# Kernel tuning notes

Measured on AMD Instinct MI355X. Metric: run time of the kernel, lower is better.

Reference implementation:

```python
import jax, jax.numpy as jnp
import numpy as np

N, E, CIN, H, B, NCOV, NCLASS, T = 50000, 800000, 64, 64, 256, 8, 2, 3


def setup_inputs() -> dict:
    key = jax.random.key(0)
    ks = jax.random.split(key, 24)
    s = 1.0 / np.sqrt(H)
    nrm = lambda k, shp, sc: (jax.random.normal(k, shp, jnp.float32) * sc)
    p = {}
    p["x"] = nrm(ks[0], (N, 3 * CIN), 1.0)
    p["edge_index"] = jax.random.randint(ks[1], (2, E), 0, N)
    p["cov"] = nrm(ks[2], (B, NCOV), 1.0)
    p["batch"] = jnp.sort(jax.random.randint(ks[3], (N,), 0, B))
    p["h0"] = nrm(ks[4], (B, H), 1.0)
    p["c0"] = nrm(ks[5], (B, H), 1.0)
    # GCNEncoder params (shared across the 3 channel slices, as in the torch code)
    p["lin_W"] = nrm(ks[6], (CIN, H), s)
    p["lin_b"] = jnp.zeros((H,), jnp.float32)
    p["conv1_W"] = nrm(ks[7], (H, H), s)
    p["conv1_b"] = jnp.zeros((H,), jnp.float32)
    p["conv2_W"] = nrm(ks[8], (H, H), s)
    p["conv2_b"] = jnp.zeros((H,), jnp.float32)
    # LSTM (1 layer), torch gate order i,f,g,o
    p["Wih"] = nrm(ks[9], (4 * H, H), s)
    p["Whh"] = nrm(ks[10], (4 * H, H), s)
    p["bih"] = jnp.zeros((4 * H,), jnp.float32)
    p["bhh"] = jnp.zeros((4 * H,), jnp.float32)
    p["w0_W"] = nrm(ks[11], (H, H), s)
    p["w0_b"] = jnp.zeros((H,), jnp.float32)
    p["attn_W"] = nrm(ks[12], (1, H), s)
    p["attn_b"] = jnp.zeros((1,), jnp.float32)
    p["l1_W"] = nrm(ks[13], (8, H), s)
    p["l1_b"] = jnp.zeros((8,), jnp.float32)
    p["l2_W"] = nrm(ks[14], (NCLASS, 8 + NCOV), 1.0 / np.sqrt(8 + NCOV))
    p["l2_b"] = jnp.zeros((NCLASS,), jnp.float32)
    return p


def _gcn_conv(x, src, dst, dinv, W, b):
    xw = x @ W
    norm = dinv[src] * dinv[dst]                      # [E]
    agg = jax.ops.segment_sum(norm[:, None] * xw[src], dst, num_segments=N)
    agg = agg + (2.0 * dinv * dinv)[:, None] * xw     # self-loop (weight 2)
    return agg + b


def _encoder(x, src, dst, dinv, lin_W, lin_b, c1W, c1b, c2W, c2b):
    out = x @ lin_W + lin_b                           # dropout = identity (eval)
    out1 = jax.nn.relu(_gcn_conv(out, src, dst, dinv, c1W, c1b)) + out
    out2 = _gcn_conv(out1, src, dst, dinv, c2W, c2b) + out1
    return out2


def reference(x, edge_index, cov, batch, h0, c0, lin_W, lin_b, conv1_W, conv1_b,
              conv2_W, conv2_b, Wih, Whh, bih, bhh, w0_W, w0_b, attn_W, attn_b,
              l1_W, l1_b, l2_W, l2_b):
    src, dst = edge_index[0], edge_index[1]
    deg = jax.ops.segment_sum(jnp.ones((E,), jnp.float32), dst, num_segments=N) + 2.0
    dinv = jax.lax.rsqrt(deg)
    enc = lambda xi: _encoder(xi, src, dst, dinv, lin_W, lin_b,
                              conv1_W, conv1_b, conv2_W, conv2_b)
    o1 = enc(x[:, :CIN]); o2 = enc(x[:, CIN:2 * CIN]); o3 = enc(x[:, 2 * CIN:])
    # global_mean_pool per branch
    cnt = jnp.maximum(jax.ops.segment_sum(jnp.ones((N,), jnp.float32), batch,
                                          num_segments=B), 1.0)[:, None]
    pool = lambda o: jax.ops.segment_sum(o, batch, num_segments=B) / cnt
    seq = jnp.stack([pool(o1), pool(o2), pool(o3)], axis=1)  # [B, 3, H]

    # 1-layer LSTM over T=3 (torch gate order i,f,g,o)
    def step(carry, x_t):
        h, c = carry
        g = x_t @ Wih.T + bih + h @ Whh.T + bhh
        i, f, gg, o = jnp.split(g, 4, axis=-1)
        c = jax.nn.sigmoid(f) * c + jax.nn.sigmoid(i) * jnp.tanh(gg)
        h = jax.nn.sigmoid(o) * jnp.tanh(c)
        return (h, c), h

    (_, _), hs = jax.lax.scan(step, (h0, c0), jnp.swapaxes(seq, 0, 1))
    rnn_out = jnp.swapaxes(hs, 0, 1)                         # [B, T, H]
    r = jnp.tanh(rnn_out @ w0_W.T + w0_b)
    attn = jax.nn.softmax((r @ attn_W.T + attn_b)[..., 0], axis=1)  # [B, T]
    pooled = jnp.einsum('bth,bt->bh', r, attn)
    out = jax.nn.relu(pooled @ l1_W.T + l1_b)
    out = jnp.concatenate([out, cov], axis=1)
    out = out @ l2_W.T + l2_b
    return attn, out
```

## Files before the change

### kernel.cpp

```cpp
#include <hip/hip_runtime.h>
#include <math.h>


#define TT 3
#define CHUNK 2048
#define BCAP 16384

typedef __attribute__((ext_vector_type(2))) float floatx2;

__device__ __forceinline__ float sigmoidf_(float x) { return 1.f / (1.f + expf(-x)); }

__global__ void brow_sorted(const int* __restrict__ batch, int* __restrict__ brow,
                            int N, int B) {
    int n = blockIdx.x * 256 + threadIdx.x;
    if (n >= N) return;
    int b = batch[n];
    if (n == 0) {
        for (int q = 0; q <= b; ++q) brow[q] = 0;
    } else {
        int pb = batch[n - 1];
        for (int q = pb + 1; q <= b; ++q) brow[q] = n;
    }
    if (n == N - 1) {
        for (int q = b + 1; q <= B; ++q) brow[q] = N;
    }
}

__global__ void stage_direct(const int* __restrict__ src, const int* __restrict__ dst,
                             int* __restrict__ bcnt, unsigned* __restrict__ stg, int E) {
    __shared__ int hcnt[256], hbase[256], hcur[256];
    hcnt[threadIdx.x] = 0;
    __syncthreads();
    int base = blockIdx.x * CHUNK;
    for (int i = threadIdx.x; i < CHUNK; i += 256) {
        int e = base + i;
        if (e < E) atomicAdd(&hcnt[dst[e] >> 8], 1);
    }
    __syncthreads();
    int c = hcnt[threadIdx.x];
    if (c) hbase[threadIdx.x] = atomicAdd(&bcnt[threadIdx.x], c);
    hcur[threadIdx.x] = 0;
    __syncthreads();
    for (int i = threadIdx.x; i < CHUNK; i += 256) {
        int e = base + i;
        if (e < E) {
            int d = dst[e];
            int b = d >> 8;
            int r = atomicAdd(&hcur[b], 1);
            stg[(long)b * BCAP + hbase[b] + r] =
                (unsigned)src[e] | ((unsigned)(d & 255) << 24);
        }
    }
}

__global__ void scan_buckets(const int* __restrict__ bcnt, int* __restrict__ boff,
                             int nb, int E) {
    __shared__ int s[256];
    int v = (threadIdx.x < nb) ? bcnt[threadIdx.x] : 0;
    s[threadIdx.x] = v;
    __syncthreads();
    for (int off = 1; off < 256; off <<= 1) {
        int t = (threadIdx.x >= off) ? s[threadIdx.x - off] : 0;
        __syncthreads();
        s[threadIdx.x] += t;
        __syncthreads();
    }
    if (threadIdx.x < nb) boff[threadIdx.x] = s[threadIdx.x] - v;
    if (threadIdx.x == 0) boff[nb] = E;
}

__global__ void bucket_build(const unsigned* __restrict__ stg, const int* __restrict__ bcnt,
                             const int* __restrict__ boff, int* __restrict__ rowptr,
                             float* __restrict__ dinv, int* __restrict__ csrc,
                             int N, int E) {
    const int b = blockIdx.x;
    const int n0 = b << 8;
    __shared__ int cnt[256];
    __shared__ int pfx[256];
    cnt[threadIdx.x] = 0;
    __syncthreads();
    const long s = (long)b * BCAP;
    const long e = s + bcnt[b];
    for (long p = s + threadIdx.x; p < e; p += 256)
        atomicAdd(&cnt[stg[p] >> 24], 1);
    __syncthreads();
    int v = cnt[threadIdx.x];
    pfx[threadIdx.x] = v;
    __syncthreads();
    for (int off = 1; off < 256; off <<= 1) {
        int t = (threadIdx.x >= off) ? pfx[threadIdx.x - off] : 0;
        __syncthreads();
        pfx[threadIdx.x] += t;
        __syncthreads();
    }
    int rowbase = boff[b] + pfx[threadIdx.x] - v;
    int n = n0 + threadIdx.x;
    if (n < N) {
        rowptr[n] = rowbase;
        dinv[n] = rsqrtf((float)v + 2.0f);
    }
    if (b == 0 && threadIdx.x == 0) rowptr[N] = E;
    cnt[threadIdx.x] = rowbase;
    __syncthreads();
    for (long p = s + threadIdx.x; p < e; p += 256) {
        unsigned u = stg[p];
        int dl = u >> 24;
        int r = atomicAdd(&cnt[dl], 1);
        csrc[r] = (int)(u & 0xFFFFFFu);
    }
}

__global__ __launch_bounds__(256) void gemm64_f32(
    const float* __restrict__ A, int lda, long aStride,
    const float* __restrict__ W, const float* __restrict__ bias,
    float* __restrict__ C, long cStride, int nrows) {
    __shared__ float AT[64][68];
    __shared__ float Ws[64][68];
    const int t = threadIdx.x;
    const float* Ab = A + (long)blockIdx.y * aStride;
    const int r0 = blockIdx.x * 64;

    #pragma unroll
    for (int i = 0; i < 4; ++i) {
        int idx = t + i * 256;
        int k = idx >> 4, c4 = idx & 15;
        *(float4*)&Ws[k][c4 * 4] = *(const float4*)(W + k * 64 + c4 * 4);
    }
    #pragma unroll
    for (int i = 0; i < 4; ++i) {
        int idx = t + i * 256;
        int row = idx >> 4, c4 = idx & 15;
        int gr = r0 + row;
        float4 a = make_float4(0.f, 0.f, 0.f, 0.f);
        if (gr < nrows) a = *(const float4*)(Ab + (long)gr * lda + c4 * 4);
        AT[c4 * 4 + 0][row] = a.x;
        AT[c4 * 4 + 1][row] = a.y;
        AT[c4 * 4 + 2][row] = a.z;
        AT[c4 * 4 + 3][row] = a.w;
    }
    __syncthreads();

    const int rowg = t >> 4, colg = t & 15;
    float acc[4][4] = {};
    #pragma unroll 8
    for (int k = 0; k < 64; ++k) {
        float4 av = *(const float4*)&AT[k][rowg * 4];
        float4 wv = *(const float4*)&Ws[k][colg * 4];
        #pragma unroll
        for (int i = 0; i < 4; ++i) {
            acc[i][0] = fmaf(((const float*)&av)[i], wv.x, acc[i][0]);
            acc[i][1] = fmaf(((const float*)&av)[i], wv.y, acc[i][1]);
            acc[i][2] = fmaf(((const float*)&av)[i], wv.z, acc[i][2]);
            acc[i][3] = fmaf(((const float*)&av)[i], wv.w, acc[i][3]);
        }
    }
    float b0 = bias[colg * 4 + 0], b1 = bias[colg * 4 + 1];
    float b2 = bias[colg * 4 + 2], b3 = bias[colg * 4 + 3];
    float* Cb = C + (long)blockIdx.y * cStride;
    #pragma unroll
    for (int i = 0; i < 4; ++i) {
        int gr = r0 + rowg * 4 + i;
        if (gr < nrows)
            *(float4*)(Cb + (long)gr * 64 + colg * 4) =
                make_float4(acc[i][0] + b0, acc[i][1] + b1, acc[i][2] + b2, acc[i][3] + b3);
    }
}

__global__ __launch_bounds__(256) void gemm64_t8(
    const float* __restrict__ A, long aStride, const float* __restrict__ W,
    unsigned* __restrict__ T8, const float* __restrict__ dinvp, int nrows) {
    __shared__ float AT[64][68];
    __shared__ float Ws[64][68];
    const int t = threadIdx.x;
    const float* Ab = A + (long)blockIdx.y * aStride;
    const int r0 = blockIdx.x * 64;

    #pragma unroll
    for (int i = 0; i < 4; ++i) {
        int idx = t + i * 256;
        int k = idx >> 4, c4 = idx & 15;
        *(float4*)&Ws[k][c4 * 4] = *(const float4*)(W + k * 64 + c4 * 4);
    }
    #pragma unroll
    for (int i = 0; i < 4; ++i) {
        int idx = t + i * 256;
        int row = idx >> 4, c4 = idx & 15;
        int gr = r0 + row;
        float4 a = make_float4(0.f, 0.f, 0.f, 0.f);
        if (gr < nrows) a = *(const float4*)(Ab + (long)gr * 64 + c4 * 4);
        AT[c4 * 4 + 0][row] = a.x;
        AT[c4 * 4 + 1][row] = a.y;
        AT[c4 * 4 + 2][row] = a.z;
        AT[c4 * 4 + 3][row] = a.w;
    }
    __syncthreads();

    const int rowg = t >> 4, colg = t & 15;
    float acc[4][4] = {};
    #pragma unroll 8
    for (int k = 0; k < 64; ++k) {
        float4 av = *(const float4*)&AT[k][rowg * 4];
        float4 wv = *(const float4*)&Ws[k][colg * 4];
        #pragma unroll
        for (int i = 0; i < 4; ++i) {
            acc[i][0] = fmaf(((const float*)&av)[i], wv.x, acc[i][0]);
            acc[i][1] = fmaf(((const float*)&av)[i], wv.y, acc[i][1]);
            acc[i][2] = fmaf(((const float*)&av)[i], wv.z, acc[i][2]);
            acc[i][3] = fmaf(((const float*)&av)[i], wv.w, acc[i][3]);
        }
    }
    #pragma unroll
    for (int i = 0; i < 4; ++i) {
        int gr = r0 + rowg * 4 + i;
        if (gr >= nrows) continue;
        float sc = dinvp[gr];
        int r = 0;
        r = __builtin_amdgcn_cvt_pk_fp8_f32(acc[i][0] * sc, acc[i][1] * sc, r, false);
        r = __builtin_amdgcn_cvt_pk_fp8_f32(acc[i][2] * sc, acc[i][3] * sc, r, true);
        T8[(long)gr * 48 + blockIdx.y * 16 + colg] = (unsigned)r;
    }
}

#define EDGE3(uu)                                                        \
    {                                                                    \
        floatx2 lo = __builtin_amdgcn_cvt_pk_f32_fp8(uu, false);         \
        floatx2 hi = __builtin_amdgcn_cvt_pk_f32_fp8(uu, true);          \
        a0[ch] += lo.x; a1[ch] += lo.y; a2[ch] += hi.x; a3[ch] += hi.y;  \
    }

template <bool RELU>
__global__ __launch_bounds__(256) void gcn_gather3_f8(
    const int* __restrict__ rowptr, const int* __restrict__ csrc,
    const float* __restrict__ dinv, const unsigned* __restrict__ tc,
    const float* __restrict__ bias, const float* __restrict__ prev, long chS,
    float* __restrict__ outp, int N) {
    long gid = ((long)blockIdx.x * 256 + threadIdx.x) >> 4;
    int n = (int)gid;
    if (n >= N) return;
    const int jj = threadIdx.x & 15;

    const int end = rowptr[n + 1];
    const float din = dinv[n];
    float a0[TT] = {}, a1[TT] = {}, a2[TT] = {}, a3[TT] = {};
    int p = rowptr[n];
    for (; p + 3 < end; p += 4) {
        long r0 = (long)csrc[p]     * 48 + jj;
        long r1 = (long)csrc[p + 1] * 48 + jj;
        long r2 = (long)csrc[p + 2] * 48 + jj;
        long r3 = (long)csrc[p + 3] * 48 + jj;
        #pragma unroll
        for (int ch = 0; ch < TT; ++ch) {
            unsigned u0 = tc[r0 + ch * 16];
            unsigned u1 = tc[r1 + ch * 16];
            unsigned u2 = tc[r2 + ch * 16];
            unsigned u3 = tc[r3 + ch * 16];
            EDGE3(u0) EDGE3(u1) EDGE3(u2) EDGE3(u3)
        }
    }
    for (; p < end; ++p) {
        long r = (long)csrc[p] * 48 + jj;
        #pragma unroll
        for (int ch = 0; ch < TT; ++ch) {
            unsigned u = tc[r + ch * 16];
            EDGE3(u)
        }
    }
    float4 bv = *(const float4*)(bias + 4 * jj);
    long nrow = (long)n * 48 + jj;
    long off = (long)n * 64 + 4 * jj;
    #pragma unroll
    for (int ch = 0; ch < TT; ++ch) {
        unsigned us = tc[nrow + ch * 16];
        floatx2 slo = __builtin_amdgcn_cvt_pk_f32_fp8(us, false);
        floatx2 shi = __builtin_amdgcn_cvt_pk_f32_fp8(us, true);
        float v0 = (a0[ch] + 2.f * slo.x) * din + bv.x;
        float v1 = (a1[ch] + 2.f * slo.y) * din + bv.y;
        float v2 = (a2[ch] + 2.f * shi.x) * din + bv.z;
        float v3 = (a3[ch] + 2.f * shi.y) * din + bv.w;
        if (RELU) {
            v0 = fmaxf(v0, 0.f); v1 = fmaxf(v1, 0.f);
            v2 = fmaxf(v2, 0.f); v3 = fmaxf(v3, 0.f);
        }
        float4 pv = *(const float4*)(prev + ch * chS + off);
        *(float4*)(outp + ch * chS + off) =
            make_float4(v0 + pv.x, v1 + pv.y, v2 + pv.z, v3 + pv.w);
    }
}

__global__ __launch_bounds__(256) void pool_range(
    const float* __restrict__ out2, long chStride, const int* __restrict__ brow,
    float* __restrict__ seq) {
    const int b = blockIdx.x;
    const int chan = blockIdx.y;
    const float* src = out2 + (long)chan * chStride;
    const int j = threadIdx.x & 63;
    const int w = threadIdx.x >> 6;
    __shared__ float part[4][64];
    float acc = 0.f;
    const int s = brow[b], e = brow[b + 1];
    for (int n = s + w; n < e; n += 4) acc += src[(long)n * 64 + j];
    part[w][j] = acc;
    __syncthreads();
    if (w == 0)
        seq[((long)b * TT + chan) * 64 + j] = part[0][j] + part[1][j] + part[2][j] + part[3][j];
}

__global__ __launch_bounds__(256) void head_kernel(
    const float* __restrict__ seq, const int* __restrict__ brow,
    const float* __restrict__ h0, const float* __restrict__ c0,
    const float* __restrict__ Wih, const float* __restrict__ Whh,
    const float* __restrict__ bih, const float* __restrict__ bhh,
    const float* __restrict__ w0W, const float* __restrict__ w0b,
    const float* __restrict__ attnW, const float* __restrict__ attnb,
    const float* __restrict__ l1W, const float* __restrict__ l1b,
    const float* __restrict__ l2W, const float* __restrict__ l2b,
    const float* __restrict__ cov, float* __restrict__ out_attn,
    float* __restrict__ out_cls) {
    const int b = blockIdx.x;
    const int t = threadIdx.x;

    __shared__ float x[TT][64];
    __shared__ float h[64], c[64];
    __shared__ float gates[256];
    __shared__ float rnn[TT][64];
    __shared__ float r[TT][64];
    __shared__ float logit[TT];
    __shared__ float a[TT];
    __shared__ float pooled[64];
    __shared__ float l1o[16];

    float inv = 1.0f / fmaxf((float)(brow[b + 1] - brow[b]), 1.0f);
    if (t < TT * 64) x[t / 64][t % 64] = seq[(long)b * TT * 64 + t] * inv;
    if (t < 64) { h[t] = h0[(long)b * 64 + t]; c[t] = c0[(long)b * 64 + t]; }
    __syncthreads();

    for (int step = 0; step < TT; ++step) {
        float g = bih[t] + bhh[t];
        const float* wi = Wih + (long)t * 64;
        const float* wh = Whh + (long)t * 64;
        #pragma unroll 8
        for (int k = 0; k < 64; ++k) g += wi[k] * x[step][k] + wh[k] * h[k];
        gates[t] = g;
        __syncthreads();
        if (t < 64) {
            float ig = sigmoidf_(gates[t]);
            float fg = sigmoidf_(gates[64 + t]);
            float gg = tanhf(gates[128 + t]);
            float og = sigmoidf_(gates[192 + t]);
            float cn = fg * c[t] + ig * gg;
            c[t] = cn;
            float hn = og * tanhf(cn);
            h[t] = hn;
            rnn[step][t] = hn;
        }
        __syncthreads();
    }

    if (t < TT * 64) {
        int tt = t / 64, j = t % 64;
        float v = w0b[j];
        const float* wr = w0W + (long)j * 64;
        #pragma unroll 8
        for (int k = 0; k < 64; ++k) v += rnn[tt][k] * wr[k];
        r[tt][j] = tanhf(v);
    }
    __syncthreads();

    if (t < TT) {
        float v = attnb[0];
        #pragma unroll 8
        for (int k = 0; k < 64; ++k) v += r[t][k] * attnW[k];
        logit[t] = v;
    }
    __syncthreads();

    if (t == 0) {
        float m = fmaxf(logit[0], fmaxf(logit[1], logit[2]));
        float e0 = expf(logit[0] - m), e1 = expf(logit[1] - m), e2 = expf(logit[2] - m);
        float s = e0 + e1 + e2;
        a[0] = e0 / s; a[1] = e1 / s; a[2] = e2 / s;
        out_attn[(long)b * TT + 0] = a[0];
        out_attn[(long)b * TT + 1] = a[1];
        out_attn[(long)b * TT + 2] = a[2];
    }
    __syncthreads();

    if (t < 64) pooled[t] = a[0] * r[0][t] + a[1] * r[1][t] + a[2] * r[2][t];
    __syncthreads();

    if (t < 8) {
        float v = l1b[t];
        const float* w = l1W + (long)t * 64;
        #pragma unroll 8
        for (int k = 0; k < 64; ++k) v += pooled[k] * w[k];
        l1o[t] = fmaxf(v, 0.f);
    } else if (t < 16) {
        l1o[t] = cov[(long)b * 8 + (t - 8)];
    }
    __syncthreads();

    if (t < 2) {
        float v = l2b[t];
        const float* w = l2W + (long)t * 16;
        #pragma unroll
        for (int k = 0; k < 16; ++k) v += l1o[k] * w[k];
        out_cls[(long)b * 2 + t] = v;
    }
}

extern "C" void kernel_launch(void* const* d_in, const int* in_sizes, int n_in,
                              void* d_out, int out_size, void* d_ws, size_t ws_size,
                              hipStream_t stream) {
    const float* x       = (const float*)d_in[0];
    const int*   eidx    = (const int*)d_in[1];
    const float* cov     = (const float*)d_in[2];
    const int*   batch   = (const int*)d_in[3];
    const float* h0      = (const float*)d_in[4];
    const float* c0      = (const float*)d_in[5];
    const float* lin_W   = (const float*)d_in[6];
    const float* lin_b   = (const float*)d_in[7];
    const float* conv1_W = (const float*)d_in[8];
    const float* conv1_b = (const float*)d_in[9];
    const float* conv2_W = (const float*)d_in[10];
    const float* conv2_b = (const float*)d_in[11];
    const float* Wih     = (const float*)d_in[12];
    const float* Whh     = (const float*)d_in[13];
    const float* bih     = (const float*)d_in[14];
    const float* bhh     = (const float*)d_in[15];
    const float* w0_W    = (const float*)d_in[16];
    const float* w0_b    = (const float*)d_in[17];
    const float* attn_W  = (const float*)d_in[18];
    const float* attn_b  = (const float*)d_in[19];
    const float* l1_W    = (const float*)d_in[20];
    const float* l1_b    = (const float*)d_in[21];
    const float* l2_W    = (const float*)d_in[22];
    const float* l2_b    = (const float*)d_in[23];

    const int N = in_sizes[3];
    const int E = in_sizes[1] / 2;
    const int B = in_sizes[2] / 8;

    const int* src = eidx;
    const int* dst = eidx + E;

    auto cdiv = [](long a, long b) { return (int)((a + b - 1) / b); };
    const int nb = cdiv(N, 256);

    char* w = (char*)d_ws;
    float* dinv   = (float*)w;  w += (size_t)N * 4;
    int*   rowptr = (int*)w;    w += (size_t)(N + 1) * 4;
    int*   brow   = (int*)w;    w += (size_t)(B + 1) * 4;
    int*   bcnt   = (int*)w;    w += 256 * 4;
    int*   boff   = (int*)w;    w += 260 * 4;
    int*   csrc   = (int*)w;    w += (size_t)E * 4;
    unsigned* stg = (unsigned*)w; w += (size_t)nb * BCAP * 4;
    float* seq    = (float*)w;  w += (size_t)B * TT * 64 * 4;
    float* buf0   = (float*)w;  w += (size_t)TT * N * 64 * 4;
    float* bufA   = (float*)w;  w += (size_t)TT * N * 64 * 4;
    unsigned* tb8 = (unsigned*)w;  w += (size_t)N * 48 * 4;
    const long chS = (long)N * 64;

    float* out_attn = (float*)d_out;
    float* out_cls  = out_attn + (long)B * TT;

    hipMemsetAsync(bcnt, 0, 256 * 4, stream);
    brow_sorted<<<cdiv(N, 256), 256, 0, stream>>>(batch, brow, N, B);
    stage_direct<<<cdiv(E, CHUNK), 256, 0, stream>>>(src, dst, bcnt, stg, E);
    scan_buckets<<<1, 256, 0, stream>>>(bcnt, boff, nb, E);
    bucket_build<<<nb, 256, 0, stream>>>(stg, bcnt, boff, rowptr, dinv, csrc, N, E);

    const int gemm_gx = cdiv(N, 64);
    const int ng_gx   = cdiv((long)N * 16, 256);

    {
        dim3 ggrid(gemm_gx, TT);
        gemm64_f32<<<ggrid, 256, 0, stream>>>(x, 3 * 64, 64, lin_W, lin_b,
                                              buf0, chS, N);
    }
    {
        dim3 ggrid(gemm_gx, TT);
        gemm64_t8<<<ggrid, 256, 0, stream>>>(buf0, chS, conv1_W, tb8, dinv, N);
    }
    gcn_gather3_f8<true><<<ng_gx, 256, 0, stream>>>(
        rowptr, csrc, dinv, tb8, conv1_b, buf0, chS, bufA, N);
    {
        dim3 ggrid(gemm_gx, TT);
        gemm64_t8<<<ggrid, 256, 0, stream>>>(bufA, chS, conv2_W, tb8, dinv, N);
    }
    gcn_gather3_f8<false><<<ng_gx, 256, 0, stream>>>(
        rowptr, csrc, dinv, tb8, conv2_b, bufA, chS, buf0, N);

    {
        dim3 pgrid(B, TT);
        pool_range<<<pgrid, 256, 0, stream>>>(buf0, chS, brow, seq);
    }

    head_kernel<<<B, 256, 0, stream>>>(seq, brow, h0, c0, Wih, Whh, bih, bhh,
                                       w0_W, w0_b, attn_W, attn_b, l1_W, l1_b,
                                       l2_W, l2_b, cov, out_attn, out_cls);
}
```

Baseline: 240.5 us.

## Store GCN activations in bf16, fuse pooling into head, fold setup kernels

Intermediate node activations (the lin output and both conv outputs) are now stored as bf16, with round-to-nearest conversion, instead of fp32. This halves the memory traffic of the GEMM and gather stages. The mean pool kernel is removed and pooling is done inside the head kernel: each thread serially sums one feature over its graph's nodes. The bucket-count memset is folded into brow_sorted, and the bucket offset scan is recomputed inside every bucket_build block, which removes two launches. The trade-offs are bf16 rounding error in the residual paths and a less parallel, longer serial pooling loop in the head kernel.

```diff
diff --git a/kernel.cpp b/kernel.cpp
--- a/kernel.cpp
+++ b/kernel.cpp
@@ -9,9 +9,18 @@
 typedef __attribute__((ext_vector_type(2))) float floatx2;
 
 __device__ __forceinline__ float sigmoidf_(float x) { return 1.f / (1.f + expf(-x)); }
+__device__ __forceinline__ float bf2f(unsigned short u) {
+    return __uint_as_float((unsigned)u << 16);
+}
+__device__ __forceinline__ unsigned short f2bf(float f) {
+    unsigned u = __float_as_uint(f);
+    u += 0x7FFFu + ((u >> 16) & 1u);
+    return (unsigned short)(u >> 16);
+}
 
 __global__ void brow_sorted(const int* __restrict__ batch, int* __restrict__ brow,
-                            int N, int B) {
+                            int* __restrict__ bcnt, int N, int B) {
+    if (blockIdx.x == 0) bcnt[threadIdx.x] = 0;
     int n = blockIdx.x * 256 + threadIdx.x;
     if (n >= N) return;
     int b = batch[n];
@@ -53,32 +62,28 @@
     }
 }
 
-__global__ void scan_buckets(const int* __restrict__ bcnt, int* __restrict__ boff,
-                             int nb, int E) {
-    __shared__ int s[256];
-    int v = (threadIdx.x < nb) ? bcnt[threadIdx.x] : 0;
-    s[threadIdx.x] = v;
-    __syncthreads();
-    for (int off = 1; off < 256; off <<= 1) {
-        int t = (threadIdx.x >= off) ? s[threadIdx.x - off] : 0;
-        __syncthreads();
-        s[threadIdx.x] += t;
-        __syncthreads();
-    }
-    if (threadIdx.x < nb) boff[threadIdx.x] = s[threadIdx.x] - v;
-    if (threadIdx.x == 0) boff[nb] = E;
-}
-
 __global__ void bucket_build(const unsigned* __restrict__ stg, const int* __restrict__ bcnt,
-                             const int* __restrict__ boff, int* __restrict__ rowptr,
-                             float* __restrict__ dinv, int* __restrict__ csrc,
-                             int N, int E) {
+                             int* __restrict__ rowptr, float* __restrict__ dinv,
+                             int* __restrict__ csrc, int nb, int N, int E) {
     const int b = blockIdx.x;
     const int n0 = b << 8;
     __shared__ int cnt[256];
     __shared__ int pfx[256];
+    __shared__ int boffb_sh;
+    int bv = (threadIdx.x < nb) ? bcnt[threadIdx.x] : 0;
+    pfx[threadIdx.x] = bv;
+    __syncthreads();
+    for (int off = 1; off < 256; off <<= 1) {
+        int t = (threadIdx.x >= off) ? pfx[threadIdx.x - off] : 0;
+        __syncthreads();
+        pfx[threadIdx.x] += t;
+        __syncthreads();
+    }
+    if (threadIdx.x == b) boffb_sh = pfx[threadIdx.x] - bv;
     cnt[threadIdx.x] = 0;
     __syncthreads();
+    const int boffb = boffb_sh;
+
     const long s = (long)b * BCAP;
     const long e = s + bcnt[b];
     for (long p = s + threadIdx.x; p < e; p += 256)
@@ -93,7 +98,7 @@
         pfx[threadIdx.x] += t;
         __syncthreads();
     }
-    int rowbase = boff[b] + pfx[threadIdx.x] - v;
+    int rowbase = boffb + pfx[threadIdx.x] - v;
     int n = n0 + threadIdx.x;
     if (n < N) {
         rowptr[n] = rowbase;
@@ -110,14 +115,13 @@
     }
 }
 
-__global__ __launch_bounds__(256) void gemm64_f32(
-    const float* __restrict__ A, int lda, long aStride,
-    const float* __restrict__ W, const float* __restrict__ bias,
-    float* __restrict__ C, long cStride, int nrows) {
+__global__ __launch_bounds__(256) void gemm_lin(
+    const float* __restrict__ x, const float* __restrict__ W,
+    const float* __restrict__ bias, unsigned short* __restrict__ C,
+    long cStride, int nrows) {
     __shared__ float AT[64][68];
     __shared__ float Ws[64][68];
     const int t = threadIdx.x;
-    const float* Ab = A + (long)blockIdx.y * aStride;
     const int r0 = blockIdx.x * 64;
 
     #pragma unroll
@@ -132,7 +136,8 @@
         int row = idx >> 4, c4 = idx & 15;
         int gr = r0 + row;
         float4 a = make_float4(0.f, 0.f, 0.f, 0.f);
-        if (gr < nrows) a = *(const float4*)(Ab + (long)gr * lda + c4 * 4);
+        if (gr < nrows)
+            a = *(const float4*)(x + (long)gr * 192 + blockIdx.y * 64 + c4 * 4);
         AT[c4 * 4 + 0][row] = a.x;
         AT[c4 * 4 + 1][row] = a.y;
         AT[c4 * 4 + 2][row] = a.z;
@@ -156,23 +161,26 @@
     }
     float b0 = bias[colg * 4 + 0], b1 = bias[colg * 4 + 1];
     float b2 = bias[colg * 4 + 2], b3 = bias[colg * 4 + 3];
-    float* Cb = C + (long)blockIdx.y * cStride;
+    unsigned short* Cb = C + (long)blockIdx.y * cStride;
     #pragma unroll
     for (int i = 0; i < 4; ++i) {
         int gr = r0 + rowg * 4 + i;
-        if (gr < nrows)
-            *(float4*)(Cb + (long)gr * 64 + colg * 4) =
-                make_float4(acc[i][0] + b0, acc[i][1] + b1, acc[i][2] + b2, acc[i][3] + b3);
-    }
-}
-
-__global__ __launch_bounds__(256) void gemm64_t8(
-    const float* __restrict__ A, long aStride, const float* __restrict__ W,
+        if (gr < nrows) {
+            ushort4 o;
+            o.x = f2bf(acc[i][0] + b0); o.y = f2bf(acc[i][1] + b1);
+            o.z = f2bf(acc[i][2] + b2); o.w = f2bf(acc[i][3] + b3);
+            *(ushort4*)(Cb + (long)gr * 64 + colg * 4) = o;
+        }
+    }
+}
+
+__global__ __launch_bounds__(256) void gemm_t8(
+    const unsigned short* __restrict__ A, long aStride, const float* __restrict__ W,
     unsigned* __restrict__ T8, const float* __restrict__ dinvp, int nrows) {
     __shared__ float AT[64][68];
     __shared__ float Ws[64][68];
     const int t = threadIdx.x;
-    const float* Ab = A + (long)blockIdx.y * aStride;
+    const unsigned short* Ab = A + (long)blockIdx.y * aStride;
     const int r0 = blockIdx.x * 64;
 
     #pragma unroll
@@ -186,12 +194,12 @@
         int idx = t + i * 256;
         int row = idx >> 4, c4 = idx & 15;
         int gr = r0 + row;
-        float4 a = make_float4(0.f, 0.f, 0.f, 0.f);
-        if (gr < nrows) a = *(const float4*)(Ab + (long)gr * 64 + c4 * 4);
-        AT[c4 * 4 + 0][row] = a.x;
-        AT[c4 * 4 + 1][row] = a.y;
-        AT[c4 * 4 + 2][row] = a.z;
-        AT[c4 * 4 + 3][row] = a.w;
+        ushort4 a = make_ushort4(0, 0, 0, 0);
+        if (gr < nrows) a = *(const ushort4*)(Ab + (long)gr * 64 + c4 * 4);
+        AT[c4 * 4 + 0][row] = bf2f(a.x);
+        AT[c4 * 4 + 1][row] = bf2f(a.y);
+        AT[c4 * 4 + 2][row] = bf2f(a.z);
+        AT[c4 * 4 + 3][row] = bf2f(a.w);
     }
     __syncthreads();
 
@@ -232,8 +240,8 @@
 __global__ __launch_bounds__(256) void gcn_gather3_f8(
     const int* __restrict__ rowptr, const int* __restrict__ csrc,
     const float* __restrict__ dinv, const unsigned* __restrict__ tc,
-    const float* __restrict__ bias, const float* __restrict__ prev, long chS,
-    float* __restrict__ outp, int N) {
+    const float* __restrict__ bias, const unsigned short* __restrict__ prev, long chS,
+    unsigned short* __restrict__ outp, int N) {
     long gid = ((long)blockIdx.x * 256 + threadIdx.x) >> 4;
     int n = (int)gid;
     if (n >= N) return;
@@ -281,32 +289,18 @@
             v0 = fmaxf(v0, 0.f); v1 = fmaxf(v1, 0.f);
             v2 = fmaxf(v2, 0.f); v3 = fmaxf(v3, 0.f);
         }
-        float4 pv = *(const float4*)(prev + ch * chS + off);
-        *(float4*)(outp + ch * chS + off) =
-            make_float4(v0 + pv.x, v1 + pv.y, v2 + pv.z, v3 + pv.w);
-    }
-}
-
-__global__ __launch_bounds__(256) void pool_range(
-    const float* __restrict__ out2, long chStride, const int* __restrict__ brow,
-    float* __restrict__ seq) {
-    const int b = blockIdx.x;
-    const int chan = blockIdx.y;
-    const float* src = out2 + (long)chan * chStride;
-    const int j = threadIdx.x & 63;
-    const int w = threadIdx.x >> 6;
-    __shared__ float part[4][64];
-    float acc = 0.f;
-    const int s = brow[b], e = brow[b + 1];
-    for (int n = s + w; n < e; n += 4) acc += src[(long)n * 64 + j];
-    part[w][j] = acc;
-    __syncthreads();
-    if (w == 0)
-        seq[((long)b * TT + chan) * 64 + j] = part[0][j] + part[1][j] + part[2][j] + part[3][j];
-}
-
-__global__ __launch_bounds__(256) void head_kernel(
-    const float* __restrict__ seq, const int* __restrict__ brow,
+        ushort4 pv = *(const ushort4*)(prev + ch * chS + off);
+        ushort4 o;
+        o.x = f2bf(v0 + bf2f(pv.x));
+        o.y = f2bf(v1 + bf2f(pv.y));
+        o.z = f2bf(v2 + bf2f(pv.z));
+        o.w = f2bf(v3 + bf2f(pv.w));
+        *(ushort4*)(outp + ch * chS + off) = o;
+    }
+}
+
+__global__ __launch_bounds__(256) void head_fused(
+    const unsigned short* __restrict__ out2, long chS, const int* __restrict__ brow,
     const float* __restrict__ h0, const float* __restrict__ c0,
     const float* __restrict__ Wih, const float* __restrict__ Whh,
     const float* __restrict__ bih, const float* __restrict__ bhh,
@@ -329,8 +323,15 @@
     __shared__ float pooled[64];
     __shared__ float l1o[16];
 
-    float inv = 1.0f / fmaxf((float)(brow[b + 1] - brow[b]), 1.0f);
-    if (t < TT * 64) x[t / 64][t % 64] = seq[(long)b * TT * 64 + t] * inv;
+    const int s = brow[b], e = brow[b + 1];
+    float inv = 1.0f / fmaxf((float)(e - s), 1.0f);
+    if (t < TT * 64) {
+        int ch = t >> 6, j = t & 63;
+        const unsigned short* p = out2 + (long)ch * chS + j;
+        float acc = 0.f;
+        for (int n = s; n < e; ++n) acc += bf2f(p[(long)n * 64]);
+        x[ch][j] = acc * inv;
+    }
     if (t < 64) { h[t] = h0[(long)b * 64 + t]; c[t] = c0[(long)b * 64 + t]; }
     __syncthreads();
 
@@ -377,8 +378,8 @@
     if (t == 0) {
         float m = fmaxf(logit[0], fmaxf(logit[1], logit[2]));
         float e0 = expf(logit[0] - m), e1 = expf(logit[1] - m), e2 = expf(logit[2] - m);
-        float s = e0 + e1 + e2;
-        a[0] = e0 / s; a[1] = e1 / s; a[2] = e2 / s;
+        float sm = e0 + e1 + e2;
+        a[0] = e0 / sm; a[1] = e1 / sm; a[2] = e2 / sm;
         out_attn[(long)b * TT + 0] = a[0];
         out_attn[(long)b * TT + 1] = a[1];
         out_attn[(long)b * TT + 2] = a[2];
@@ -451,51 +452,41 @@
     int*   rowptr = (int*)w;    w += (size_t)(N + 1) * 4;
     int*   brow   = (int*)w;    w += (size_t)(B + 1) * 4;
     int*   bcnt   = (int*)w;    w += 256 * 4;
-    int*   boff   = (int*)w;    w += 260 * 4;
     int*   csrc   = (int*)w;    w += (size_t)E * 4;
     unsigned* stg = (unsigned*)w; w += (size_t)nb * BCAP * 4;
-    float* seq    = (float*)w;  w += (size_t)B * TT * 64 * 4;
-    float* buf0   = (float*)w;  w += (size_t)TT * N * 64 * 4;
-    float* bufA   = (float*)w;  w += (size_t)TT * N * 64 * 4;
+    unsigned short* buf0 = (unsigned short*)w;  w += (size_t)TT * N * 64 * 2;
+    unsigned short* bufA = (unsigned short*)w;  w += (size_t)TT * N * 64 * 2;
     unsigned* tb8 = (unsigned*)w;  w += (size_t)N * 48 * 4;
     const long chS = (long)N * 64;
 
     float* out_attn = (float*)d_out;
     float* out_cls  = out_attn + (long)B * TT;
 
-    hipMemsetAsync(bcnt, 0, 256 * 4, stream);
-    brow_sorted<<<cdiv(N, 256), 256, 0, stream>>>(batch, brow, N, B);
+    brow_sorted<<<cdiv(N, 256), 256, 0, stream>>>(batch, brow, bcnt, N, B);
     stage_direct<<<cdiv(E, CHUNK), 256, 0, stream>>>(src, dst, bcnt, stg, E);
-    scan_buckets<<<1, 256, 0, stream>>>(bcnt, boff, nb, E);
-    bucket_build<<<nb, 256, 0, stream>>>(stg, bcnt, boff, rowptr, dinv, csrc, N, E);
+    bucket_build<<<nb, 256, 0, stream>>>(stg, bcnt, rowptr, dinv, csrc, nb, N, E);
 
     const int gemm_gx = cdiv(N, 64);
     const int ng_gx   = cdiv((long)N * 16, 256);
 
     {
         dim3 ggrid(gemm_gx, TT);
-        gemm64_f32<<<ggrid, 256, 0, stream>>>(x, 3 * 64, 64, lin_W, lin_b,
-                                              buf0, chS, N);
+        gemm_lin<<<ggrid, 256, 0, stream>>>(x, lin_W, lin_b, buf0, chS, N);
     }
     {
         dim3 ggrid(gemm_gx, TT);
-        gemm64_t8<<<ggrid, 256, 0, stream>>>(buf0, chS, conv1_W, tb8, dinv, N);
+        gemm_t8<<<ggrid, 256, 0, stream>>>(buf0, chS, conv1_W, tb8, dinv, N);
     }
     gcn_gather3_f8<true><<<ng_gx, 256, 0, stream>>>(
         rowptr, csrc, dinv, tb8, conv1_b, buf0, chS, bufA, N);
     {
         dim3 ggrid(gemm_gx, TT);
-        gemm64_t8<<<ggrid, 256, 0, stream>>>(bufA, chS, conv2_W, tb8, dinv, N);
+        gemm_t8<<<ggrid, 256, 0, stream>>>(bufA, chS, conv2_W, tb8, dinv, N);
     }
     gcn_gather3_f8<false><<<ng_gx, 256, 0, stream>>>(
         rowptr, csrc, dinv, tb8, conv2_b, bufA, chS, buf0, N);
 
-    {
-        dim3 pgrid(B, TT);
-        pool_range<<<pgrid, 256, 0, stream>>>(buf0, chS, brow, seq);
-    }
-
-    head_kernel<<<B, 256, 0, stream>>>(seq, brow, h0, c0, Wih, Whh, bih, bhh,
-                                       w0_W, w0_b, attn_W, attn_b, l1_W, l1_b,
-                                       l2_W, l2_b, cov, out_attn, out_cls);
-}
+    head_fused<<<B, 256, 0, stream>>>(buf0, chS, brow, h0, c0, Wih, Whh, bih, bhh,
+                                      w0_W, w0_b, attn_W, attn_b, l1_W, l1_b,
+                                      l2_W, l2_b, cov, out_attn, out_cls);
+}
```

New measurement: 258.9 us. 7.6% more time.
